# Optimization experiments

Measured on AMD Instinct MI355X. Metric: run time of the kernel, lower is better.

Reference implementation:

```python
import jax, jax.numpy as jnp
import numpy as np

N, E, D, L, G = 50000, 1600000, 128, 3, 64


def setup_inputs() -> dict:
    key = jax.random.key(0)
    ks = jax.random.split(key, 10)
    s = 1.0 / np.sqrt(D).astype(np.float32)
    X = jax.random.normal(ks[0], (N, D), jnp.float32)
    edge_index = jax.random.randint(ks[1], (2, E), 0, N, dtype=jnp.int32)
    edge_types = jax.random.randint(ks[2], (E,), 0, 2, dtype=jnp.int32)
    batch_ids = jnp.sort(jax.random.randint(ks[3], (N,), 0, G, dtype=jnp.int32))
    Wd = jax.random.uniform(ks[4], (L, D, D), jnp.float32, -s, s)
    bd = jax.random.uniform(ks[5], (L, D), jnp.float32, -s, s)
    Wc = jax.random.uniform(ks[6], (L, D, D), jnp.float32, -s, s)
    bc = jax.random.uniform(ks[7], (L, D), jnp.float32, -s, s)
    Ws = jax.random.uniform(ks[8], (L, D, D), jnp.float32, -s, s)
    bs = jax.random.uniform(ks[9], (L, D), jnp.float32, -s, s)
    return dict(X=X, Wd=Wd, bd=bd, Wc=Wc, bc=bc, Ws=Ws, bs=bs,
                edge_index=edge_index, edge_types=edge_types, batch_ids=batch_ids)


def reference(X, Wd, bd, Wc, bc, Ws, bs, edge_index, edge_types, batch_ids):
    src, dst = edge_index[0], edge_index[1]
    is_data = (edge_types == 0)[:, None]  # [E,1] edge-type selector
    for l in range(L):
        # Linear commutes with gather: compute node-level GEMMs once,
        # then per-edge gather + type select (same math as per-edge Linear).
        Xd = X @ Wd[l] + bd[l]            # [N,D] data-edge messages
        Xc = X @ Wc[l] + bc[l]            # [N,D] control-edge messages
        msg = jnp.where(is_data, Xd[src], Xc[src])      # [E,D]
        agg = jax.ops.segment_sum(msg, dst, num_segments=N)  # scatter-add
        X = jax.nn.relu(agg + X @ Ws[l] + bs[l])
    # global mean pool per graph
    sums = jax.ops.segment_sum(X, batch_ids, num_segments=G)
    cnts = jax.ops.segment_sum(jnp.ones((N,), X.dtype), batch_ids, num_segments=G)
    return sums / jnp.maximum(cnts, 1.0)[:, None]
```

## Files before the change

kernel.cpp:

```cpp
#include <hip/hip_runtime.h>
#include <hip/hip_fp16.h>

#define N_NODES 50000
#define N_EDGES 1600000
#define DIM     128
#define NLAYERS 3
#define NGRAPHS 64

#define NBUCK   196
#define CSR_BLKS 256
#define EPB     (N_EDGES / CSR_BLKS)
#define EITER   ((EPB + 255) / 256)

typedef _Float16 half8 __attribute__((ext_vector_type(8)));
typedef float    f32x4 __attribute__((ext_vector_type(4)));
typedef float    f32x2 __attribute__((ext_vector_type(2)));

#define LDK 136

__device__ __forceinline__ unsigned char f32_to_fp8(float v) {
    int q = __builtin_amdgcn_cvt_pk_fp8_f32(v, v, 0, false);
    return (unsigned char)(q & 0xFF);
}

__global__ __launch_bounds__(256) void setup_kernel(
        const float* __restrict__ X, __half* __restrict__ Xh,
        const float* __restrict__ Wd, const float* __restrict__ Wc,
        const float* __restrict__ Ws, __half* __restrict__ WT,
        float* __restrict__ sums, int* __restrict__ gcnt) {
    int i = blockIdx.x * 256 + threadIdx.x;
    if (i < N_NODES * DIM / 4) {
        float4 v = *(const float4*)(X + (size_t)i * 4);
        union { __half2 h2[2]; uint2 u; } pk;
        pk.h2[0] = __floats2half2_rn(v.x, v.y);
        pk.h2[1] = __floats2half2_rn(v.z, v.w);
        *(uint2*)(Xh + (size_t)i * 4) = pk.u;
    }
    if (i < 9 * DIM * DIM) {
        int k  = i & 127;
        int n  = (i >> 7) & 127;
        int lw = i >> 14;
        int l  = lw / 3, w = lw - 3 * l;
        const float* W = ((w == 0) ? Wd : (w == 1) ? Wc : Ws)
                         + (size_t)l * DIM * DIM;
        WT[i] = __float2half(W[k * DIM + n]);
    }
    if (i < NGRAPHS * DIM) sums[i] = 0.f;
    if (i < NGRAPHS) gcnt[i] = 0;
}

__global__ __launch_bounds__(256) void csr1_kernel(const int* __restrict__ dst,
                                                   int* __restrict__ cntmat) {
    __shared__ int hc[NBUCK];
    int tid = threadIdx.x;
    for (int i = tid; i < NBUCK; i += 256) hc[i] = 0;
    __syncthreads();
    int base = blockIdx.x * EPB;
#pragma unroll
    for (int i = 0; i < EITER; ++i) {
        int idx = i * 256 + tid;
        if (idx < EPB) atomicAdd(&hc[dst[base + idx] >> 8], 1);
    }
    __syncthreads();
    for (int i = tid; i < NBUCK; i += 256)
        cntmat[i * CSR_BLKS + blockIdx.x] = hc[i];
}

__global__ __launch_bounds__(256) void scanA_kernel(const int* __restrict__ cntmat,
                                                    int* __restrict__ exc,
                                                    int* __restrict__ btot) {
    __shared__ int sh[256];
    int tid = threadIdx.x, b = blockIdx.x;
    int v = cntmat[b * CSR_BLKS + tid];
    sh[tid] = v;
    __syncthreads();
    for (int o = 1; o < 256; o <<= 1) {
        int t = (tid >= o) ? sh[tid - o] : 0;
        __syncthreads();
        sh[tid] += t;
        __syncthreads();
    }
    exc[b * CSR_BLKS + tid] = sh[tid] - v;
    if (tid == 255) btot[b] = sh[255];
}

__global__ __launch_bounds__(256) void csr2_kernel(const int* __restrict__ src,
                                                   const int* __restrict__ dst,
                                                   const int* __restrict__ et,
                                                   const int* __restrict__ exc,
                                                   const int* __restrict__ btot,
                                                   int* __restrict__ bstart,
                                                   int* __restrict__ esv) {
    __shared__ int sh[256];
    __shared__ int bst[NBUCK];
    __shared__ int cur[NBUCK];
    int tid = threadIdx.x;
    int v = (tid < NBUCK) ? btot[tid] : 0;
    sh[tid] = v;
    __syncthreads();
    for (int o = 1; o < 256; o <<= 1) {
        int t = (tid >= o) ? sh[tid - o] : 0;
        __syncthreads();
        sh[tid] += t;
        __syncthreads();
    }
    if (tid < NBUCK) bst[tid] = sh[tid] - v;
    if (blockIdx.x == 0) {
        if (tid < NBUCK) bstart[tid] = sh[tid] - v;
        if (tid == NBUCK - 1) bstart[NBUCK] = sh[tid];
    }
    __syncthreads();
    if (tid < NBUCK) cur[tid] = exc[tid * CSR_BLKS + blockIdx.x] + bst[tid];
    __syncthreads();
    int base = blockIdx.x * EPB;
#pragma unroll
    for (int i = 0; i < EITER; ++i) {
        int idx = i * 256 + tid;
        if (idx < EPB) {
            int e = base + idx;
            int d = dst[e];
            int pos = atomicAdd(&cur[d >> 8], 1);
            esv[pos] = (src[e] + et[e] * N_NODES) | ((d & 255) << 17);
        }
    }
}

__global__ __launch_bounds__(256) void csr3_kernel(const int* __restrict__ esv,
                                                   const int* __restrict__ bstart,
                                                   int* __restrict__ col,
                                                   int* __restrict__ row_start,
                                                   int* __restrict__ deg) {
    __shared__ int cnt[256];
    __shared__ int sh[256];
    __shared__ int cur[256];
    int tid = threadIdx.x, b = blockIdx.x;
    int bs = bstart[b], be = bstart[b + 1];
    cnt[tid] = 0;
    __syncthreads();
    for (int e = bs + tid; e < be; e += 256)
        atomicAdd(&cnt[(esv[e] >> 17) & 255], 1);
    __syncthreads();
    int v = cnt[tid];
    sh[tid] = v;
    __syncthreads();
    for (int o = 1; o < 256; o <<= 1) {
        int t = (tid >= o) ? sh[tid - o] : 0;
        __syncthreads();
        sh[tid] += t;
        __syncthreads();
    }
    int off  = sh[tid] - v;
    int node = (b << 8) + tid;
    if (node < N_NODES) {
        row_start[node] = bs + off;
        deg[node]       = v;
    }
    cur[tid] = bs + off;
    __syncthreads();
    for (int e = bs + tid; e < be; e += 256) {
        int pk  = esv[e];
        int nd  = (pk >> 17) & 255;
        int pos = atomicAdd(&cur[nd], 1);
        col[pos] = pk & 0x1FFFF;
    }
}

__global__ __launch_bounds__(256) void gemm3m_kernel(
        const __half* __restrict__ Xh,
        const __half* __restrict__ WTl,
        const float* __restrict__ bd, const float* __restrict__ bc,
        const float* __restrict__ bs,
        unsigned char* __restrict__ Od, unsigned char* __restrict__ Oc,
        __half* __restrict__ Sh) {
    __shared__ _Float16 As[64 * LDK];
    __shared__ _Float16 Bs[128 * LDK];

    const int tid = threadIdx.x;
    const int m0  = blockIdx.x * 64;
    const int w   = blockIdx.y;

#pragma unroll
    for (int i = 0; i < 4; ++i) {
        int c    = i * 256 + tid;
        int row  = c >> 4;
        int colh = (c & 15) * 8;
        uint4 v  = make_uint4(0u, 0u, 0u, 0u);
        int gr   = m0 + row;
        if (gr < N_NODES) v = *(const uint4*)(Xh + (size_t)gr * DIM + colh);
        *(uint4*)(As + row * LDK + colh) = v;
    }
    {
        const __half* Wt = WTl + (size_t)w * DIM * DIM;
#pragma unroll
        for (int i = 0; i < 8; ++i) {
            int c    = i * 256 + tid;
            int row  = c >> 4;
            int colh = (c & 15) * 8;
            uint4 v = *(const uint4*)(Wt + (size_t)row * DIM + colh);
            *(uint4*)(Bs + row * LDK + colh) = v;
        }
    }
    __syncthreads();

    const int wv = tid >> 6;
    const int l  = tid & 63;
    const int lm = l & 15;
    const int q  = l >> 4;

    const float* bias = (w == 0) ? bd : (w == 1) ? bc : bs;
    float b0v = bias[wv * 32 + lm];
    float b1v = bias[wv * 32 + 16 + lm];
    f32x4 acc[4][2];
#pragma unroll
    for (int mt = 0; mt < 4; ++mt) {
        acc[mt][0] = (f32x4){b0v, b0v, b0v, b0v};
        acc[mt][1] = (f32x4){b1v, b1v, b1v, b1v};
    }

#pragma unroll
    for (int ks = 0; ks < 4; ++ks) {
        int coff = ks * 32 + q * 8;
        half8 am[4];
#pragma unroll
        for (int mt = 0; mt < 4; ++mt)
            am[mt] = *(const half8*)(As + (mt * 16 + lm) * LDK + coff);
        half8 bb0 = *(const half8*)(Bs + (wv * 32 + lm) * LDK + coff);
        half8 bb1 = *(const half8*)(Bs + (wv * 32 + 16 + lm) * LDK + coff);
#pragma unroll
        for (int mt = 0; mt < 4; ++mt) {
            acc[mt][0] = __builtin_amdgcn_mfma_f32_16x16x32_f16(am[mt], bb0, acc[mt][0], 0, 0, 0);
            acc[mt][1] = __builtin_amdgcn_mfma_f32_16x16x32_f16(am[mt], bb1, acc[mt][1], 0, 0, 0);
        }
    }

    if (w < 2) {
        unsigned char* O = (w == 0) ? Od : Oc;
#pragma unroll
        for (int mt = 0; mt < 4; ++mt)
#pragma unroll
            for (int nt = 0; nt < 2; ++nt) {
                int colg = wv * 32 + nt * 16 + lm;
#pragma unroll
                for (int r = 0; r < 4; ++r) {
                    int row = m0 + mt * 16 + q * 4 + r;
                    if (row < N_NODES)
                        O[(size_t)row * DIM + colg] = f32_to_fp8(acc[mt][nt][r]);
                }
            }
    } else {
#pragma unroll
        for (int mt = 0; mt < 4; ++mt)
#pragma unroll
            for (int nt = 0; nt < 2; ++nt) {
                int colg = wv * 32 + nt * 16 + lm;
#pragma unroll
                for (int r = 0; r < 4; ++r) {
                    int row = m0 + mt * 16 + q * 4 + r;
                    if (row < N_NODES)
                        Sh[(size_t)row * DIM + colg] = __float2half(acc[mt][nt][r]);
                }
            }
    }
}

__global__ __launch_bounds__(256) void agg_kernel(
        const int* __restrict__ row_start, const int* __restrict__ deg_arr,
        const int* __restrict__ col,
        const unsigned char* __restrict__ Xdc,
        const __half* __restrict__ Sh, __half* __restrict__ Xout) {
    int wave = (blockIdx.x * 256 + threadIdx.x) >> 6;
    int lane = threadIdx.x & 63;
    int grp  = lane >> 4;
    int l16  = lane & 15;
    int node = wave * 4 + grp;
    if (node >= N_NODES) return;

    int rs  = row_start[node];
    int deg = deg_arr[node];
    const size_t off = (size_t)l16 * 8;

    union { uint4 u; __half2 h2[4]; } sv;
    sv.u = *(const uint4*)(Sh + (size_t)node * DIM + off);

    float acc[8];
#pragma unroll
    for (int j = 0; j < 8; ++j) acc[j] = 0.f;

    if (deg > 0) {
        int dgm1 = deg - 1;
        int nb   = (deg + 7) >> 3;
        int p[8];
#pragma unroll
        for (int i = 0; i < 8; ++i)
            p[i] = col[rs + (i < deg ? i : dgm1)];
        for (int b = 0; b < nb; ++b) {
            int e0 = b * 8;
            uint2 v[8];
#pragma unroll
            for (int i = 0; i < 8; ++i)
                v[i] = *(const uint2*)(Xdc + (size_t)p[i] * DIM + off);
            int pn[8];
            if (b + 1 < nb) {
                int e1 = e0 + 8;
#pragma unroll
                for (int i = 0; i < 8; ++i) {
                    int idx = e1 + i;
                    pn[i] = col[rs + (idx < deg ? idx : dgm1)];
                }
            }
#pragma unroll
            for (int i = 0; i < 8; ++i) {
                if (e0 + i >= deg) { v[i].x = 0u; v[i].y = 0u; }
            }
#pragma unroll
            for (int i = 0; i < 8; ++i) {
                f32x2 f0 = __builtin_amdgcn_cvt_pk_f32_fp8(v[i].x, false);
                f32x2 f1 = __builtin_amdgcn_cvt_pk_f32_fp8(v[i].x, true);
                f32x2 f2 = __builtin_amdgcn_cvt_pk_f32_fp8(v[i].y, false);
                f32x2 f3 = __builtin_amdgcn_cvt_pk_f32_fp8(v[i].y, true);
                acc[0] += f0[0]; acc[1] += f0[1];
                acc[2] += f1[0]; acc[3] += f1[1];
                acc[4] += f2[0]; acc[5] += f2[1];
                acc[6] += f3[0]; acc[7] += f3[1];
            }
            if (b + 1 < nb) {
#pragma unroll
                for (int i = 0; i < 8; ++i) p[i] = pn[i];
            }
        }
    }

    float s[8];
#pragma unroll
    for (int j = 0; j < 4; ++j) {
        float2 f = __half22float2(sv.h2[j]);
        s[2 * j]     = f.x;
        s[2 * j + 1] = f.y;
    }

    union { __half2 h2[4]; uint4 u; } pk;
#pragma unroll
    for (int j = 0; j < 4; ++j) {
        float r0 = fmaxf(acc[2 * j]     + s[2 * j],     0.f);
        float r1 = fmaxf(acc[2 * j + 1] + s[2 * j + 1], 0.f);
        pk.h2[j] = __floats2half2_rn(r0, r1);
    }
    *(uint4*)(Xout + (size_t)node * DIM + off) = pk.u;
}

__global__ __launch_bounds__(256) void pool_kernel(const __half* __restrict__ X,
                                                   const int* __restrict__ bid,
                                                   float* __restrict__ sums,
                                                   int* __restrict__ gcnt) {
    __shared__ float acc[8][DIM];
    __shared__ int scnt[8];
    __shared__ int sgmin;
    int tid = threadIdx.x;
    for (int i = tid; i < 8 * DIM; i += 256) ((float*)acc)[i] = 0.f;
    if (tid < 8) scnt[tid] = 0;
    int n0 = blockIdx.x * 64;
    if (tid == 0) sgmin = bid[n0];
    __syncthreads();
    int gmin = sgmin;

    int s    = tid >> 5;
    int lane = tid & 31;
    int r0   = n0 + s * 8;

    int g[8];
    union { uint2 u; __half2 h2[2]; } v[8];
#pragma unroll
    for (int i = 0; i < 8; ++i) {
        int r = r0 + i;
        g[i] = (r < N_NODES) ? bid[r] : -1;
    }
#pragma unroll
    for (int i = 0; i < 8; ++i) {
        int r = r0 + i;
        if (r < N_NODES)
            v[i].u = *(const uint2*)(X + (size_t)r * DIM + lane * 4);
        else { v[i].u.x = 0u; v[i].u.y = 0u; }
    }

    float4 a = make_float4(0.f, 0.f, 0.f, 0.f);
    int cur = -1, run = 0;
#pragma unroll
    for (int i = 0; i < 8; ++i) {
        if (g[i] != cur) {
            if (cur >= 0) {
                int slot = cur - gmin;
                if (slot < 8) {
                    atomicAdd(&acc[slot][lane * 4 + 0], a.x);
                    atomicAdd(&acc[slot][lane * 4 + 1], a.y);
                    atomicAdd(&acc[slot][lane * 4 + 2], a.z);
                    atomicAdd(&acc[slot][lane * 4 + 3], a.w);
                    if (lane == 0) atomicAdd(&scnt[slot], run);
                } else {
                    atomicAdd(&sums[cur * DIM + lane * 4 + 0], a.x);
                    atomicAdd(&sums[cur * DIM + lane * 4 + 1], a.y);
                    atomicAdd(&sums[cur * DIM + lane * 4 + 2], a.z);
                    atomicAdd(&sums[cur * DIM + lane * 4 + 3], a.w);
                    if (lane == 0) atomicAdd(&gcnt[cur], run);
                }
            }
            cur = g[i];
            a = make_float4(0.f, 0.f, 0.f, 0.f);
            run = 0;
        }
        if (g[i] >= 0) {
            float2 f0 = __half22float2(v[i].h2[0]);
            float2 f1 = __half22float2(v[i].h2[1]);
            a.x += f0.x; a.y += f0.y; a.z += f1.x; a.w += f1.y;
            run++;
        }
    }
    if (cur >= 0) {
        int slot = cur - gmin;
        if (slot < 8) {
            atomicAdd(&acc[slot][lane * 4 + 0], a.x);
            atomicAdd(&acc[slot][lane * 4 + 1], a.y);
            atomicAdd(&acc[slot][lane * 4 + 2], a.z);
            atomicAdd(&acc[slot][lane * 4 + 3], a.w);
            if (lane == 0) atomicAdd(&scnt[slot], run);
        } else {
            atomicAdd(&sums[cur * DIM + lane * 4 + 0], a.x);
            atomicAdd(&sums[cur * DIM + lane * 4 + 1], a.y);
            atomicAdd(&sums[cur * DIM + lane * 4 + 2], a.z);
            atomicAdd(&sums[cur * DIM + lane * 4 + 3], a.w);
            if (lane == 0) atomicAdd(&gcnt[cur], run);
        }
    }
    __syncthreads();

    for (int slot = 0; slot < 8; ++slot) {
        if (scnt[slot] > 0) {
            int gg = gmin + slot;
            for (int i = tid; i < DIM; i += 256)
                atomicAdd(&sums[gg * DIM + i], acc[slot][i]);
            if (tid == 0) atomicAdd(&gcnt[gg], scnt[slot]);
        }
    }
}

__global__ __launch_bounds__(256) void div_kernel(const float* __restrict__ sums,
                                                  const int* __restrict__ gcnt,
                                                  float* __restrict__ out) {
    int i = blockIdx.x * 256 + threadIdx.x;
    if (i < NGRAPHS * DIM) {
        int g = i >> 7;
        out[i] = sums[i] / fmaxf((float)gcnt[g], 1.f);
    }
}

extern "C" void kernel_launch(void* const* d_in, const int* in_sizes, int n_in,
                              void* d_out, int out_size, void* d_ws, size_t ws_size,
                              hipStream_t stream) {
    const float* Xin = (const float*)d_in[0];
    const float* Wd  = (const float*)d_in[1];
    const float* bd  = (const float*)d_in[2];
    const float* Wc  = (const float*)d_in[3];
    const float* bc  = (const float*)d_in[4];
    const float* Ws  = (const float*)d_in[5];
    const float* bs  = (const float*)d_in[6];
    const int* edge_index = (const int*)d_in[7];
    const int* edge_types = (const int*)d_in[8];
    const int* batch_ids  = (const int*)d_in[9];

    const int* src = edge_index;
    const int* dst = edge_index + N_EDGES;

    const size_t NBH = (size_t)N_NODES * DIM * sizeof(__half);
    const size_t NB8 = (size_t)N_NODES * DIM;
    char* w = (char*)d_ws;
    auto take = [&](size_t bytes) {
        char* p = w;
        w += (bytes + 255) & ~(size_t)255;
        return p;
    };
    __half* X0h  = (__half*)take(NBH);
    __half* Xb0h = (__half*)take(NBH);
    __half* Xb1h = (__half*)take(NBH);
    unsigned char* Xdc = (unsigned char*)take(2 * NB8);
    __half* Shb  = (__half*)take(NBH);
    __half* WT   = (__half*)take((size_t)9 * DIM * DIM * sizeof(__half));
    int* col     = (int*)take((size_t)N_EDGES * 4);
    int* esv     = (int*)take((size_t)N_EDGES * 4);
    int* cntmat  = (int*)take((size_t)NBUCK * CSR_BLKS * 4);
    int* exc     = (int*)take((size_t)NBUCK * CSR_BLKS * 4);
    int* btot    = (int*)take((size_t)NBUCK * 4);
    int* bstart  = (int*)take((size_t)(NBUCK + 1) * 4);
    int* rowst   = (int*)take((size_t)N_NODES * 4);
    int* deg     = (int*)take((size_t)N_NODES * 4);
    float* sums  = (float*)take((size_t)NGRAPHS * DIM * 4);
    int* gcnt    = (int*)take(NGRAPHS * 4);

    setup_kernel<<<(N_NODES * DIM / 4 + 255) / 256, 256, 0, stream>>>(
        Xin, X0h, Wd, Wc, Ws, WT, sums, gcnt);

    csr1_kernel<<<CSR_BLKS, 256, 0, stream>>>(dst, cntmat);
    scanA_kernel<<<NBUCK, 256, 0, stream>>>(cntmat, exc, btot);
    csr2_kernel<<<CSR_BLKS, 256, 0, stream>>>(src, dst, edge_types, exc,
                                              btot, bstart, esv);
    csr3_kernel<<<NBUCK, 256, 0, stream>>>(esv, bstart, col, rowst, deg);

    const int GEMM_MBLK = (N_NODES + 63) / 64;
    const int AGG_BLKS  = (N_NODES + 15) / 16;
    const __half* Xcur = X0h;
    __half* bufs[3] = {Xb0h, Xb1h, Xb0h};
    for (int l = 0; l < NLAYERS; ++l) {
        gemm3m_kernel<<<dim3(GEMM_MBLK, 3), 256, 0, stream>>>(
            Xcur, WT + (size_t)l * 3 * DIM * DIM,
            bd + (size_t)l * DIM, bc + (size_t)l * DIM, bs + (size_t)l * DIM,
            Xdc, Xdc + NB8, Shb);
        __half* Xnext = bufs[l];
        agg_kernel<<<AGG_BLKS, 256, 0, stream>>>(rowst, deg, col, Xdc, Shb, Xnext);
        Xcur = Xnext;
    }

    const int POOL_BLKS = (N_NODES + 63) / 64;
    pool_kernel<<<POOL_BLKS, 256, 0, stream>>>(Xcur, batch_ids, sums, gcnt);
    div_kernel<<<(NGRAPHS * DIM + 255) / 256, 256, 0, stream>>>(sums, gcnt,
                                                                (float*)d_out);
}
```

Measured before the change: 307.2 us.

## Fuse fp32-to-fp16 input conversion into GEMM and compute all three weights per block

The separate setup pass that converts X from fp32 to fp16 is removed, and the first layer's GEMM now reads fp32 X directly and converts it while filling shared memory. The GEMM grid drops its weight dimension, so each block loads its A tile once and loops over the three weight matrices, reloading B each time. This cuts the redundant A-tile global loads, the fp16 copy of X, and one pass over memory. In exchange each block runs longer with fewer blocks in flight, and adds a barrier between weight matrices.

```diff
diff --git a/kernel.cpp b/kernel.cpp
--- a/kernel.cpp
+++ b/kernel.cpp
@@ -24,18 +24,10 @@
 }
 
 __global__ __launch_bounds__(256) void setup_kernel(
-        const float* __restrict__ X, __half* __restrict__ Xh,
         const float* __restrict__ Wd, const float* __restrict__ Wc,
         const float* __restrict__ Ws, __half* __restrict__ WT,
         float* __restrict__ sums, int* __restrict__ gcnt) {
     int i = blockIdx.x * 256 + threadIdx.x;
-    if (i < N_NODES * DIM / 4) {
-        float4 v = *(const float4*)(X + (size_t)i * 4);
-        union { __half2 h2[2]; uint2 u; } pk;
-        pk.h2[0] = __floats2half2_rn(v.x, v.y);
-        pk.h2[1] = __floats2half2_rn(v.z, v.w);
-        *(uint2*)(Xh + (size_t)i * 4) = pk.u;
-    }
     if (i < 9 * DIM * DIM) {
         int k  = i & 127;
         int n  = (i >> 7) & 127;
@@ -166,7 +158,8 @@
 }
 
 __global__ __launch_bounds__(256) void gemm3m_kernel(
-        const __half* __restrict__ Xh,
+        const void* __restrict__ Xin_,
+        int a_fp32,
         const __half* __restrict__ WTl,
         const float* __restrict__ bd, const float* __restrict__ bc,
         const float* __restrict__ bs,
@@ -177,89 +170,110 @@
 
     const int tid = threadIdx.x;
     const int m0  = blockIdx.x * 64;
-    const int w   = blockIdx.y;
-
-#pragma unroll
-    for (int i = 0; i < 4; ++i) {
-        int c    = i * 256 + tid;
-        int row  = c >> 4;
-        int colh = (c & 15) * 8;
-        uint4 v  = make_uint4(0u, 0u, 0u, 0u);
-        int gr   = m0 + row;
-        if (gr < N_NODES) v = *(const uint4*)(Xh + (size_t)gr * DIM + colh);
-        *(uint4*)(As + row * LDK + colh) = v;
-    }
-    {
-        const __half* Wt = WTl + (size_t)w * DIM * DIM;
+
+    if (a_fp32) {
+        const float* Xf = (const float*)Xin_;
 #pragma unroll
         for (int i = 0; i < 8; ++i) {
+            int c    = i * 256 + tid;
+            int row  = c >> 5;
+            int col4 = (c & 31) * 4;
+            int gr   = m0 + row;
+            float4 v = make_float4(0.f, 0.f, 0.f, 0.f);
+            if (gr < N_NODES) v = *(const float4*)(Xf + (size_t)gr * DIM + col4);
+            union { __half2 h2[2]; uint2 u; } pk;
+            pk.h2[0] = __floats2half2_rn(v.x, v.y);
+            pk.h2[1] = __floats2half2_rn(v.z, v.w);
+            *(uint2*)(As + row * LDK + col4) = pk.u;
+        }
+    } else {
+        const __half* Xh = (const __half*)Xin_;
+#pragma unroll
+        for (int i = 0; i < 4; ++i) {
             int c    = i * 256 + tid;
             int row  = c >> 4;
             int colh = (c & 15) * 8;
-            uint4 v = *(const uint4*)(Wt + (size_t)row * DIM + colh);
-            *(uint4*)(Bs + row * LDK + colh) = v;
-        }
-    }
-    __syncthreads();
+            uint4 v  = make_uint4(0u, 0u, 0u, 0u);
+            int gr   = m0 + row;
+            if (gr < N_NODES) v = *(const uint4*)(Xh + (size_t)gr * DIM + colh);
+            *(uint4*)(As + row * LDK + colh) = v;
+        }
+    }
 
     const int wv = tid >> 6;
     const int l  = tid & 63;
     const int lm = l & 15;
     const int q  = l >> 4;
 
-    const float* bias = (w == 0) ? bd : (w == 1) ? bc : bs;
-    float b0v = bias[wv * 32 + lm];
-    float b1v = bias[wv * 32 + 16 + lm];
-    f32x4 acc[4][2];
-#pragma unroll
-    for (int mt = 0; mt < 4; ++mt) {
-        acc[mt][0] = (f32x4){b0v, b0v, b0v, b0v};
-        acc[mt][1] = (f32x4){b1v, b1v, b1v, b1v};
-    }
-
-#pragma unroll
-    for (int ks = 0; ks < 4; ++ks) {
-        int coff = ks * 32 + q * 8;
-        half8 am[4];
-#pragma unroll
-        for (int mt = 0; mt < 4; ++mt)
-            am[mt] = *(const half8*)(As + (mt * 16 + lm) * LDK + coff);
-        half8 bb0 = *(const half8*)(Bs + (wv * 32 + lm) * LDK + coff);
-        half8 bb1 = *(const half8*)(Bs + (wv * 32 + 16 + lm) * LDK + coff);
+    for (int w = 0; w < 3; ++w) {
+        if (w) __syncthreads();
+        {
+            const __half* Wt = WTl + (size_t)w * DIM * DIM;
+#pragma unroll
+            for (int i = 0; i < 8; ++i) {
+                int c    = i * 256 + tid;
+                int row  = c >> 4;
+                int colh = (c & 15) * 8;
+                uint4 v = *(const uint4*)(Wt + (size_t)row * DIM + colh);
+                *(uint4*)(Bs + row * LDK + colh) = v;
+            }
+        }
+        __syncthreads();
+
+        const float* bias = (w == 0) ? bd : (w == 1) ? bc : bs;
+        float b0v = bias[wv * 32 + lm];
+        float b1v = bias[wv * 32 + 16 + lm];
+        f32x4 acc[4][2];
 #pragma unroll
         for (int mt = 0; mt < 4; ++mt) {
-            acc[mt][0] = __builtin_amdgcn_mfma_f32_16x16x32_f16(am[mt], bb0, acc[mt][0], 0, 0, 0);
-            acc[mt][1] = __builtin_amdgcn_mfma_f32_16x16x32_f16(am[mt], bb1, acc[mt][1], 0, 0, 0);
-        }
-    }
-
-    if (w < 2) {
-        unsigned char* O = (w == 0) ? Od : Oc;
-#pragma unroll
-        for (int mt = 0; mt < 4; ++mt)
-#pragma unroll
-            for (int nt = 0; nt < 2; ++nt) {
-                int colg = wv * 32 + nt * 16 + lm;
-#pragma unroll
-                for (int r = 0; r < 4; ++r) {
-                    int row = m0 + mt * 16 + q * 4 + r;
-                    if (row < N_NODES)
-                        O[(size_t)row * DIM + colg] = f32_to_fp8(acc[mt][nt][r]);
+            acc[mt][0] = (f32x4){b0v, b0v, b0v, b0v};
+            acc[mt][1] = (f32x4){b1v, b1v, b1v, b1v};
+        }
+
+#pragma unroll
+        for (int ks = 0; ks < 4; ++ks) {
+            int coff = ks * 32 + q * 8;
+            half8 am[4];
+#pragma unroll
+            for (int mt = 0; mt < 4; ++mt)
+                am[mt] = *(const half8*)(As + (mt * 16 + lm) * LDK + coff);
+            half8 bb0 = *(const half8*)(Bs + (wv * 32 + lm) * LDK + coff);
+            half8 bb1 = *(const half8*)(Bs + (wv * 32 + 16 + lm) * LDK + coff);
+#pragma unroll
+            for (int mt = 0; mt < 4; ++mt) {
+                acc[mt][0] = __builtin_amdgcn_mfma_f32_16x16x32_f16(am[mt], bb0, acc[mt][0], 0, 0, 0);
+                acc[mt][1] = __builtin_amdgcn_mfma_f32_16x16x32_f16(am[mt], bb1, acc[mt][1], 0, 0, 0);
+            }
+        }
+
+        if (w < 2) {
+            unsigned char* O = (w == 0) ? Od : Oc;
+#pragma unroll
+            for (int mt = 0; mt < 4; ++mt)
+#pragma unroll
+                for (int nt = 0; nt < 2; ++nt) {
+                    int colg = wv * 32 + nt * 16 + lm;
+#pragma unroll
+                    for (int r = 0; r < 4; ++r) {
+                        int row = m0 + mt * 16 + q * 4 + r;
+                        if (row < N_NODES)
+                            O[(size_t)row * DIM + colg] = f32_to_fp8(acc[mt][nt][r]);
+                    }
                 }
-            }
-    } else {
-#pragma unroll
-        for (int mt = 0; mt < 4; ++mt)
-#pragma unroll
-            for (int nt = 0; nt < 2; ++nt) {
-                int colg = wv * 32 + nt * 16 + lm;
-#pragma unroll
-                for (int r = 0; r < 4; ++r) {
-                    int row = m0 + mt * 16 + q * 4 + r;
-                    if (row < N_NODES)
-                        Sh[(size_t)row * DIM + colg] = __float2half(acc[mt][nt][r]);
+        } else {
+#pragma unroll
+            for (int mt = 0; mt < 4; ++mt)
+#pragma unroll
+                for (int nt = 0; nt < 2; ++nt) {
+                    int colg = wv * 32 + nt * 16 + lm;
+#pragma unroll
+                    for (int r = 0; r < 4; ++r) {
+                        int row = m0 + mt * 16 + q * 4 + r;
+                        if (row < N_NODES)
+                            Sh[(size_t)row * DIM + colg] = __float2half(acc[mt][nt][r]);
+                    }
                 }
-            }
+        }
     }
 }
 
@@ -477,7 +491,6 @@
         w += (bytes + 255) & ~(size_t)255;
         return p;
     };
-    __half* X0h  = (__half*)take(NBH);
     __half* Xb0h = (__half*)take(NBH);
     __half* Xb1h = (__half*)take(NBH);
     unsigned char* Xdc = (unsigned char*)take(2 * NB8);
@@ -494,8 +507,8 @@
     float* sums  = (float*)take((size_t)NGRAPHS * DIM * 4);
     int* gcnt    = (int*)take(NGRAPHS * 4);
 
-    setup_kernel<<<(N_NODES * DIM / 4 + 255) / 256, 256, 0, stream>>>(
-        Xin, X0h, Wd, Wc, Ws, WT, sums, gcnt);
+    setup_kernel<<<(9 * DIM * DIM + 255) / 256, 256, 0, stream>>>(
+        Wd, Wc, Ws, WT, sums, gcnt);
 
     csr1_kernel<<<CSR_BLKS, 256, 0, stream>>>(dst, cntmat);
     scanA_kernel<<<NBUCK, 256, 0, stream>>>(cntmat, exc, btot);
@@ -505,20 +518,23 @@
 
     const int GEMM_MBLK = (N_NODES + 63) / 64;
     const int AGG_BLKS  = (N_NODES + 15) / 16;
-    const __half* Xcur = X0h;
+    const void* Xcur = (const void*)Xin;
+    int a_fp32 = 1;
     __half* bufs[3] = {Xb0h, Xb1h, Xb0h};
     for (int l = 0; l < NLAYERS; ++l) {
-        gemm3m_kernel<<<dim3(GEMM_MBLK, 3), 256, 0, stream>>>(
-            Xcur, WT + (size_t)l * 3 * DIM * DIM,
+        gemm3m_kernel<<<GEMM_MBLK, 256, 0, stream>>>(
+            Xcur, a_fp32, WT + (size_t)l * 3 * DIM * DIM,
             bd + (size_t)l * DIM, bc + (size_t)l * DIM, bs + (size_t)l * DIM,
             Xdc, Xdc + NB8, Shb);
         __half* Xnext = bufs[l];
         agg_kernel<<<AGG_BLKS, 256, 0, stream>>>(rowst, deg, col, Xdc, Shb, Xnext);
-        Xcur = Xnext;
+        Xcur = (const void*)Xnext;
+        a_fp32 = 0;
     }
 
     const int POOL_BLKS = (N_NODES + 63) / 64;
-    pool_kernel<<<POOL_BLKS, 256, 0, stream>>>(Xcur, batch_ids, sums, gcnt);
+    pool_kernel<<<POOL_BLKS, 256, 0, stream>>>((const __half*)Xcur, batch_ids,
+                                               sums, gcnt);
     div_kernel<<<(NGRAPHS * DIM + 255) / 256, 256, 0, stream>>>(sums, gcnt,
                                                                 (float*)d_out);
 }
```

New measurement: 307.4 us. About the same (+0.1%).

## Aggregate raw node features before GEMM and fuse three projections into one kernel

Applied to the files above, without the earlier changes.

Reorders each layer so aggregation runs first over fp8 copies of the node features, producing per-type neighbor sums (data and control), then a fused GEMM kernel multiplies those sums and X by Wd, Wc, Ws and accumulates into one result. Biases are applied through per-node data/control degree counts that csr3 now computes. The gather reads one fp8 row per edge instead of a type-offset row from a doubled message buffer, and the separate 3-way GEMM launch plus skip buffer round trip are merged. In exchange the aggregation does twice the fp8 conversions and accumulations, writes two fp16 sum buffers, and the fp8 quantization now hits the inputs rather than the messages, which changes numerical error.

```diff
diff --git a/kernel.cpp b/kernel.cpp
--- a/kernel.cpp
+++ b/kernel.cpp
@@ -25,6 +25,7 @@
 
 __global__ __launch_bounds__(256) void setup_kernel(
         const float* __restrict__ X, __half* __restrict__ Xh,
+        unsigned char* __restrict__ X8,
         const float* __restrict__ Wd, const float* __restrict__ Wc,
         const float* __restrict__ Ws, __half* __restrict__ WT,
         float* __restrict__ sums, int* __restrict__ gcnt) {
@@ -35,6 +36,9 @@
         pk.h2[0] = __floats2half2_rn(v.x, v.y);
         pk.h2[1] = __floats2half2_rn(v.z, v.w);
         *(uint2*)(Xh + (size_t)i * 4) = pk.u;
+        int q0 = __builtin_amdgcn_cvt_pk_fp8_f32(v.x, v.y, 0, false);
+        int q1 = __builtin_amdgcn_cvt_pk_fp8_f32(v.z, v.w, q0, true);
+        *(unsigned int*)(X8 + (size_t)i * 4) = (unsigned int)q1;
     }
     if (i < 9 * DIM * DIM) {
         int k  = i & 127;
@@ -129,16 +133,23 @@
                                                    const int* __restrict__ bstart,
                                                    int* __restrict__ col,
                                                    int* __restrict__ row_start,
-                                                   int* __restrict__ deg) {
+                                                   int* __restrict__ deg,
+                                                   int* __restrict__ degd) {
     __shared__ int cnt[256];
+    __shared__ int cntd[256];
     __shared__ int sh[256];
     __shared__ int cur[256];
     int tid = threadIdx.x, b = blockIdx.x;
     int bs = bstart[b], be = bstart[b + 1];
     cnt[tid] = 0;
-    __syncthreads();
-    for (int e = bs + tid; e < be; e += 256)
-        atomicAdd(&cnt[(esv[e] >> 17) & 255], 1);
+    cntd[tid] = 0;
+    __syncthreads();
+    for (int e = bs + tid; e < be; e += 256) {
+        int pk = esv[e];
+        int nd = (pk >> 17) & 255;
+        atomicAdd(&cnt[nd], 1);
+        if ((pk & 0x1FFFF) < N_NODES) atomicAdd(&cntd[nd], 1);
+    }
     __syncthreads();
     int v = cnt[tid];
     sh[tid] = v;
@@ -154,6 +165,7 @@
     if (node < N_NODES) {
         row_start[node] = bs + off;
         deg[node]       = v;
+        degd[node]      = cntd[tid];
     }
     cur[tid] = bs + off;
     __syncthreads();
@@ -165,109 +177,11 @@
     }
 }
 
-__global__ __launch_bounds__(256) void gemm3m_kernel(
-        const __half* __restrict__ Xh,
-        const __half* __restrict__ WTl,
-        const float* __restrict__ bd, const float* __restrict__ bc,
-        const float* __restrict__ bs,
-        unsigned char* __restrict__ Od, unsigned char* __restrict__ Oc,
-        __half* __restrict__ Sh) {
-    __shared__ _Float16 As[64 * LDK];
-    __shared__ _Float16 Bs[128 * LDK];
-
-    const int tid = threadIdx.x;
-    const int m0  = blockIdx.x * 64;
-    const int w   = blockIdx.y;
-
-#pragma unroll
-    for (int i = 0; i < 4; ++i) {
-        int c    = i * 256 + tid;
-        int row  = c >> 4;
-        int colh = (c & 15) * 8;
-        uint4 v  = make_uint4(0u, 0u, 0u, 0u);
-        int gr   = m0 + row;
-        if (gr < N_NODES) v = *(const uint4*)(Xh + (size_t)gr * DIM + colh);
-        *(uint4*)(As + row * LDK + colh) = v;
-    }
-    {
-        const __half* Wt = WTl + (size_t)w * DIM * DIM;
-#pragma unroll
-        for (int i = 0; i < 8; ++i) {
-            int c    = i * 256 + tid;
-            int row  = c >> 4;
-            int colh = (c & 15) * 8;
-            uint4 v = *(const uint4*)(Wt + (size_t)row * DIM + colh);
-            *(uint4*)(Bs + row * LDK + colh) = v;
-        }
-    }
-    __syncthreads();
-
-    const int wv = tid >> 6;
-    const int l  = tid & 63;
-    const int lm = l & 15;
-    const int q  = l >> 4;
-
-    const float* bias = (w == 0) ? bd : (w == 1) ? bc : bs;
-    float b0v = bias[wv * 32 + lm];
-    float b1v = bias[wv * 32 + 16 + lm];
-    f32x4 acc[4][2];
-#pragma unroll
-    for (int mt = 0; mt < 4; ++mt) {
-        acc[mt][0] = (f32x4){b0v, b0v, b0v, b0v};
-        acc[mt][1] = (f32x4){b1v, b1v, b1v, b1v};
-    }
-
-#pragma unroll
-    for (int ks = 0; ks < 4; ++ks) {
-        int coff = ks * 32 + q * 8;
-        half8 am[4];
-#pragma unroll
-        for (int mt = 0; mt < 4; ++mt)
-            am[mt] = *(const half8*)(As + (mt * 16 + lm) * LDK + coff);
-        half8 bb0 = *(const half8*)(Bs + (wv * 32 + lm) * LDK + coff);
-        half8 bb1 = *(const half8*)(Bs + (wv * 32 + 16 + lm) * LDK + coff);
-#pragma unroll
-        for (int mt = 0; mt < 4; ++mt) {
-            acc[mt][0] = __builtin_amdgcn_mfma_f32_16x16x32_f16(am[mt], bb0, acc[mt][0], 0, 0, 0);
-            acc[mt][1] = __builtin_amdgcn_mfma_f32_16x16x32_f16(am[mt], bb1, acc[mt][1], 0, 0, 0);
-        }
-    }
-
-    if (w < 2) {
-        unsigned char* O = (w == 0) ? Od : Oc;
-#pragma unroll
-        for (int mt = 0; mt < 4; ++mt)
-#pragma unroll
-            for (int nt = 0; nt < 2; ++nt) {
-                int colg = wv * 32 + nt * 16 + lm;
-#pragma unroll
-                for (int r = 0; r < 4; ++r) {
-                    int row = m0 + mt * 16 + q * 4 + r;
-                    if (row < N_NODES)
-                        O[(size_t)row * DIM + colg] = f32_to_fp8(acc[mt][nt][r]);
-                }
-            }
-    } else {
-#pragma unroll
-        for (int mt = 0; mt < 4; ++mt)
-#pragma unroll
-            for (int nt = 0; nt < 2; ++nt) {
-                int colg = wv * 32 + nt * 16 + lm;
-#pragma unroll
-                for (int r = 0; r < 4; ++r) {
-                    int row = m0 + mt * 16 + q * 4 + r;
-                    if (row < N_NODES)
-                        Sh[(size_t)row * DIM + colg] = __float2half(acc[mt][nt][r]);
-                }
-            }
-    }
-}
-
 __global__ __launch_bounds__(256) void agg_kernel(
         const int* __restrict__ row_start, const int* __restrict__ deg_arr,
         const int* __restrict__ col,
-        const unsigned char* __restrict__ Xdc,
-        const __half* __restrict__ Sh, __half* __restrict__ Xout) {
+        const unsigned char* __restrict__ X8,
+        __half* __restrict__ Sd, __half* __restrict__ Sc) {
     int wave = (blockIdx.x * 256 + threadIdx.x) >> 6;
     int lane = threadIdx.x & 63;
     int grp  = lane >> 4;
@@ -279,12 +193,9 @@
     int deg = deg_arr[node];
     const size_t off = (size_t)l16 * 8;
 
-    union { uint4 u; __half2 h2[4]; } sv;
-    sv.u = *(const uint4*)(Sh + (size_t)node * DIM + off);
-
-    float acc[8];
-#pragma unroll
-    for (int j = 0; j < 8; ++j) acc[j] = 0.f;
+    float aT[8], aD[8];
+#pragma unroll
+    for (int j = 0; j < 8; ++j) { aT[j] = 0.f; aD[j] = 0.f; }
 
     if (deg > 0) {
         int dgm1 = deg - 1;
@@ -296,9 +207,15 @@
         for (int b = 0; b < nb; ++b) {
             int e0 = b * 8;
             uint2 v[8];
-#pragma unroll
-            for (int i = 0; i < 8; ++i)
-                v[i] = *(const uint2*)(Xdc + (size_t)p[i] * DIM + off);
+            int  c[8];
+#pragma unroll
+            for (int i = 0; i < 8; ++i) {
+                int pi  = p[i];
+                int isC = pi >= N_NODES;
+                int row = pi - (isC ? N_NODES : 0);
+                c[i] = isC;
+                v[i] = *(const uint2*)(X8 + (size_t)row * DIM + off);
+            }
             int pn[8];
             if (b + 1 < nb) {
                 int e1 = e0 + 8;
@@ -314,14 +231,24 @@
             }
 #pragma unroll
             for (int i = 0; i < 8; ++i) {
-                f32x2 f0 = __builtin_amdgcn_cvt_pk_f32_fp8(v[i].x, false);
-                f32x2 f1 = __builtin_amdgcn_cvt_pk_f32_fp8(v[i].x, true);
-                f32x2 f2 = __builtin_amdgcn_cvt_pk_f32_fp8(v[i].y, false);
-                f32x2 f3 = __builtin_amdgcn_cvt_pk_f32_fp8(v[i].y, true);
-                acc[0] += f0[0]; acc[1] += f0[1];
-                acc[2] += f1[0]; acc[3] += f1[1];
-                acc[4] += f2[0]; acc[5] += f2[1];
-                acc[6] += f3[0]; acc[7] += f3[1];
+                unsigned int dx = c[i] ? 0u : v[i].x;
+                unsigned int dy = c[i] ? 0u : v[i].y;
+                f32x2 t0 = __builtin_amdgcn_cvt_pk_f32_fp8(v[i].x, false);
+                f32x2 t1 = __builtin_amdgcn_cvt_pk_f32_fp8(v[i].x, true);
+                f32x2 t2 = __builtin_amdgcn_cvt_pk_f32_fp8(v[i].y, false);
+                f32x2 t3 = __builtin_amdgcn_cvt_pk_f32_fp8(v[i].y, true);
+                aT[0] += t0[0]; aT[1] += t0[1];
+                aT[2] += t1[0]; aT[3] += t1[1];
+                aT[4] += t2[0]; aT[5] += t2[1];
+                aT[6] += t3[0]; aT[7] += t3[1];
+                f32x2 d0 = __builtin_amdgcn_cvt_pk_f32_fp8(dx, false);
+                f32x2 d1 = __builtin_amdgcn_cvt_pk_f32_fp8(dx, true);
+                f32x2 d2 = __builtin_amdgcn_cvt_pk_f32_fp8(dy, false);
+                f32x2 d3 = __builtin_amdgcn_cvt_pk_f32_fp8(dy, true);
+                aD[0] += d0[0]; aD[1] += d0[1];
+                aD[2] += d1[0]; aD[3] += d1[1];
+                aD[4] += d2[0]; aD[5] += d2[1];
+                aD[6] += d3[0]; aD[7] += d3[1];
             }
             if (b + 1 < nb) {
 #pragma unroll
@@ -330,22 +257,111 @@
         }
     }
 
-    float s[8];
+    union { __half2 h2[4]; uint4 u; } pd, pc;
 #pragma unroll
     for (int j = 0; j < 4; ++j) {
-        float2 f = __half22float2(sv.h2[j]);
-        s[2 * j]     = f.x;
-        s[2 * j + 1] = f.y;
-    }
-
-    union { __half2 h2[4]; uint4 u; } pk;
-#pragma unroll
-    for (int j = 0; j < 4; ++j) {
-        float r0 = fmaxf(acc[2 * j]     + s[2 * j],     0.f);
-        float r1 = fmaxf(acc[2 * j + 1] + s[2 * j + 1], 0.f);
-        pk.h2[j] = __floats2half2_rn(r0, r1);
-    }
-    *(uint4*)(Xout + (size_t)node * DIM + off) = pk.u;
+        pd.h2[j] = __floats2half2_rn(aD[2 * j], aD[2 * j + 1]);
+        pc.h2[j] = __floats2half2_rn(aT[2 * j] - aD[2 * j],
+                                     aT[2 * j + 1] - aD[2 * j + 1]);
+    }
+    *(uint4*)(Sd + (size_t)node * DIM + off) = pd.u;
+    *(uint4*)(Sc + (size_t)node * DIM + off) = pc.u;
+}
+
+__global__ __launch_bounds__(256) void gemm_fused_kernel(
+        const __half* __restrict__ Sd, const __half* __restrict__ Sc,
+        const __half* __restrict__ Xh,
+        const __half* __restrict__ WTl,
+        const float* __restrict__ bd, const float* __restrict__ bc,
+        const float* __restrict__ bs,
+        const int* __restrict__ degd, const int* __restrict__ deg,
+        __half* __restrict__ Xh_out, unsigned char* __restrict__ X8_out,
+        int write8) {
+    __shared__ _Float16 As[64 * LDK];
+    __shared__ _Float16 Bs[128 * LDK];
+
+    const int tid = threadIdx.x;
+    const int m0  = blockIdx.x * 64;
+
+    const int wv = tid >> 6;
+    const int l  = tid & 63;
+    const int lm = l & 15;
+    const int q  = l >> 4;
+
+    f32x4 acc[4][2];
+#pragma unroll
+    for (int mt = 0; mt < 4; ++mt) {
+        acc[mt][0] = (f32x4){0.f, 0.f, 0.f, 0.f};
+        acc[mt][1] = (f32x4){0.f, 0.f, 0.f, 0.f};
+    }
+
+    for (int w = 0; w < 3; ++w) {
+        if (w) __syncthreads();
+        const __half* Asrc = (w == 0) ? Sd : (w == 1) ? Sc : Xh;
+#pragma unroll
+        for (int i = 0; i < 4; ++i) {
+            int c    = i * 256 + tid;
+            int row  = c >> 4;
+            int colh = (c & 15) * 8;
+            uint4 v  = make_uint4(0u, 0u, 0u, 0u);
+            int gr   = m0 + row;
+            if (gr < N_NODES) v = *(const uint4*)(Asrc + (size_t)gr * DIM + colh);
+            *(uint4*)(As + row * LDK + colh) = v;
+        }
+        {
+            const __half* Wt = WTl + (size_t)w * DIM * DIM;
+#pragma unroll
+            for (int i = 0; i < 8; ++i) {
+                int c    = i * 256 + tid;
+                int row  = c >> 4;
+                int colh = (c & 15) * 8;
+                uint4 v = *(const uint4*)(Wt + (size_t)row * DIM + colh);
+                *(uint4*)(Bs + row * LDK + colh) = v;
+            }
+        }
+        __syncthreads();
+
+#pragma unroll
+        for (int ks = 0; ks < 4; ++ks) {
+            int coff = ks * 32 + q * 8;
+            half8 am[4];
+#pragma unroll
+            for (int mt = 0; mt < 4; ++mt)
+                am[mt] = *(const half8*)(As + (mt * 16 + lm) * LDK + coff);
+            half8 bb0 = *(const half8*)(Bs + (wv * 32 + lm) * LDK + coff);
+            half8 bb1 = *(const half8*)(Bs + (wv * 32 + 16 + lm) * LDK + coff);
+#pragma unroll
+            for (int mt = 0; mt < 4; ++mt) {
+                acc[mt][0] = __builtin_amdgcn_mfma_f32_16x16x32_f16(am[mt], bb0, acc[mt][0], 0, 0, 0);
+                acc[mt][1] = __builtin_amdgcn_mfma_f32_16x16x32_f16(am[mt], bb1, acc[mt][1], 0, 0, 0);
+            }
+        }
+    }
+
+    const int colg0 = wv * 32 + lm;
+    const int colg1 = wv * 32 + 16 + lm;
+    float bd0 = bd[colg0], bd1 = bd[colg1];
+    float bc0 = bc[colg0], bc1 = bc[colg1];
+    float bs0 = bs[colg0], bs1 = bs[colg1];
+#pragma unroll
+    for (int mt = 0; mt < 4; ++mt) {
+#pragma unroll
+        for (int r = 0; r < 4; ++r) {
+            int row = m0 + mt * 16 + q * 4 + r;
+            if (row < N_NODES) {
+                float dd = (float)degd[row];
+                float dc = (float)(deg[row] - degd[row]);
+                float v0 = fmaxf(acc[mt][0][r] + dd * bd0 + dc * bc0 + bs0, 0.f);
+                float v1 = fmaxf(acc[mt][1][r] + dd * bd1 + dc * bc1 + bs1, 0.f);
+                Xh_out[(size_t)row * DIM + colg0] = __float2half(v0);
+                Xh_out[(size_t)row * DIM + colg1] = __float2half(v1);
+                if (write8) {
+                    X8_out[(size_t)row * DIM + colg0] = f32_to_fp8(v0);
+                    X8_out[(size_t)row * DIM + colg1] = f32_to_fp8(v1);
+                }
+            }
+        }
+    }
 }
 
 __global__ __launch_bounds__(256) void pool_kernel(const __half* __restrict__ X,
@@ -477,11 +493,12 @@
         w += (bytes + 255) & ~(size_t)255;
         return p;
     };
-    __half* X0h  = (__half*)take(NBH);
-    __half* Xb0h = (__half*)take(NBH);
-    __half* Xb1h = (__half*)take(NBH);
-    unsigned char* Xdc = (unsigned char*)take(2 * NB8);
-    __half* Shb  = (__half*)take(NBH);
+    __half* Xh0  = (__half*)take(NBH);
+    __half* Xh1  = (__half*)take(NBH);
+    unsigned char* X8a = (unsigned char*)take(NB8);
+    unsigned char* X8b = (unsigned char*)take(NB8);
+    __half* SdB  = (__half*)take(NBH);
+    __half* ScB  = (__half*)take(NBH);
     __half* WT   = (__half*)take((size_t)9 * DIM * DIM * sizeof(__half));
     int* col     = (int*)take((size_t)N_EDGES * 4);
     int* esv     = (int*)take((size_t)N_EDGES * 4);
@@ -491,34 +508,38 @@
     int* bstart  = (int*)take((size_t)(NBUCK + 1) * 4);
     int* rowst   = (int*)take((size_t)N_NODES * 4);
     int* deg     = (int*)take((size_t)N_NODES * 4);
+    int* degd    = (int*)take((size_t)N_NODES * 4);
     float* sums  = (float*)take((size_t)NGRAPHS * DIM * 4);
     int* gcnt    = (int*)take(NGRAPHS * 4);
 
     setup_kernel<<<(N_NODES * DIM / 4 + 255) / 256, 256, 0, stream>>>(
-        Xin, X0h, Wd, Wc, Ws, WT, sums, gcnt);
+        Xin, Xh0, X8a, Wd, Wc, Ws, WT, sums, gcnt);
 
     csr1_kernel<<<CSR_BLKS, 256, 0, stream>>>(dst, cntmat);
     scanA_kernel<<<NBUCK, 256, 0, stream>>>(cntmat, exc, btot);
     csr2_kernel<<<CSR_BLKS, 256, 0, stream>>>(src, dst, edge_types, exc,
                                               btot, bstart, esv);
-    csr3_kernel<<<NBUCK, 256, 0, stream>>>(esv, bstart, col, rowst, deg);
+    csr3_kernel<<<NBUCK, 256, 0, stream>>>(esv, bstart, col, rowst, deg, degd);
 
     const int GEMM_MBLK = (N_NODES + 63) / 64;
     const int AGG_BLKS  = (N_NODES + 15) / 16;
-    const __half* Xcur = X0h;
-    __half* bufs[3] = {Xb0h, Xb1h, Xb0h};
+
+    const __half*      Xhc = Xh0;
+    const unsigned char* X8c = X8a;
+    __half*            XhN[3] = {Xh1, Xh0, Xh1};
+    unsigned char*     X8N[3] = {X8b, X8a, X8b};
     for (int l = 0; l < NLAYERS; ++l) {
-        gemm3m_kernel<<<dim3(GEMM_MBLK, 3), 256, 0, stream>>>(
-            Xcur, WT + (size_t)l * 3 * DIM * DIM,
+        agg_kernel<<<AGG_BLKS, 256, 0, stream>>>(rowst, deg, col, X8c, SdB, ScB);
+        gemm_fused_kernel<<<GEMM_MBLK, 256, 0, stream>>>(
+            SdB, ScB, Xhc, WT + (size_t)l * 3 * DIM * DIM,
             bd + (size_t)l * DIM, bc + (size_t)l * DIM, bs + (size_t)l * DIM,
-            Xdc, Xdc + NB8, Shb);
-        __half* Xnext = bufs[l];
-        agg_kernel<<<AGG_BLKS, 256, 0, stream>>>(rowst, deg, col, Xdc, Shb, Xnext);
-        Xcur = Xnext;
+            degd, deg, XhN[l], X8N[l], (l < NLAYERS - 1) ? 1 : 0);
+        Xhc = XhN[l];
+        X8c = X8N[l];
     }
 
     const int POOL_BLKS = (N_NODES + 63) / 64;
-    pool_kernel<<<POOL_BLKS, 256, 0, stream>>>(Xcur, batch_ids, sums, gcnt);
+    pool_kernel<<<POOL_BLKS, 256, 0, stream>>>(Xhc, batch_ids, sums, gcnt);
     div_kernel<<<(NGRAPHS * DIM + 255) / 256, 256, 0, stream>>>(sums, gcnt,
                                                                 (float*)d_out);
 }
```

Measured after the change: 335.1 us. 1.09x slower.
